# Performance work log

Hardware: AMD Instinct MI355X
Metric: run time of the kernel (lower is better)

Reference implementation:

```python
import jax, jax.numpy as jnp
import numpy as np

B, T, D_IN = 1024, 512, 32   # batch, sequence_length, input_dim
H = 512                      # hidden_dim
P = 96                       # prediction_length
D_OUT = 1                    # output_dim


def setup_inputs() -> dict:
    key = jax.random.key(0)
    ks = jax.random.split(key, 24)
    s = 1.0 / np.sqrt(H)  # PyTorch GRU default init scale
    u = lambda k, shape: jax.random.uniform(k, shape, jnp.float32, -s, s)
    inp = {"x": jax.random.normal(ks[0], (B, T, D_IN), jnp.float32)}
    # Encoder GRU: layer0 input D_IN, layer1 input H. Gate order: r, z, n.
    inp["enc_Wih0"] = u(ks[1], (3 * H, D_IN)); inp["enc_Whh0"] = u(ks[2], (3 * H, H))
    inp["enc_bih0"] = u(ks[3], (3 * H,));      inp["enc_bhh0"] = u(ks[4], (3 * H,))
    inp["enc_Wih1"] = u(ks[5], (3 * H, H));    inp["enc_Whh1"] = u(ks[6], (3 * H, H))
    inp["enc_bih1"] = u(ks[7], (3 * H,));      inp["enc_bhh1"] = u(ks[8], (3 * H,))
    # Decoder GRU: layer0 input D_OUT, layer1 input H.
    inp["dec_Wih0"] = u(ks[9], (3 * H, D_OUT)); inp["dec_Whh0"] = u(ks[10], (3 * H, H))
    inp["dec_bih0"] = u(ks[11], (3 * H,));      inp["dec_bhh0"] = u(ks[12], (3 * H,))
    inp["dec_Wih1"] = u(ks[13], (3 * H, H));    inp["dec_Whh1"] = u(ks[14], (3 * H, H))
    inp["dec_bih1"] = u(ks[15], (3 * H,));      inp["dec_bhh1"] = u(ks[16], (3 * H,))
    # Output projection + learned decoder start token.
    inp["out_W"] = u(ks[17], (D_OUT, H)); inp["out_b"] = u(ks[18], (D_OUT,))
    inp["dec_start"] = jnp.zeros((1, 1, D_OUT), jnp.float32)
    return inp


def gru_cell(x, h, Wih, Whh, bih, bhh):
    # PyTorch GRU cell: r,z,n gate order.
    gi = x @ Wih.T + bih          # [B, 3H]
    gh = h @ Whh.T + bhh          # [B, 3H]
    ir, iz, inn = jnp.split(gi, 3, axis=-1)
    hr, hz, hn = jnp.split(gh, 3, axis=-1)
    r = jax.nn.sigmoid(ir + hr)
    z = jax.nn.sigmoid(iz + hz)
    n = jnp.tanh(inn + r * hn)
    return (1.0 - z) * n + z * h


def reference(x,
              enc_Wih0, enc_Whh0, enc_bih0, enc_bhh0,
              enc_Wih1, enc_Whh1, enc_bih1, enc_bhh1,
              dec_Wih0, dec_Whh0, dec_bih0, dec_bhh0,
              dec_Wih1, dec_Whh1, dec_bih1, dec_bhh1,
              out_W, out_b, dec_start):
    Bsz = x.shape[0]
    h0 = jnp.zeros((Bsz, H), x.dtype)

    def enc_step(carry, xt):
        h1, h2 = carry
        h1 = gru_cell(xt, h1, enc_Wih0, enc_Whh0, enc_bih0, enc_bhh0)
        h2 = gru_cell(h1, h2, enc_Wih1, enc_Whh1, enc_bih1, enc_bhh1)
        return (h1, h2), None

    (h1, h2), _ = jax.lax.scan(enc_step, (h0, h0), jnp.swapaxes(x, 0, 1))

    y0 = jnp.broadcast_to(dec_start[0], (Bsz, D_OUT)).astype(x.dtype)

    def dec_step(carry, _):
        d1, d2, y = carry
        d1 = gru_cell(y, d1, dec_Wih0, dec_Whh0, dec_bih0, dec_bhh0)
        d2 = gru_cell(d1, d2, dec_Wih1, dec_Whh1, dec_bih1, dec_bhh1)
        y = d2 @ out_W.T + out_b  # [B, D_OUT]
        return (d1, d2, y), y

    _, ys = jax.lax.scan(dec_step, (h1, h2, y0), None, length=P)
    return jnp.swapaxes(ys, 0, 1)  # [B, P, D_OUT]
```

## Files before the change

### kernel.cpp

```cpp
#include <hip/hip_runtime.h>

#define HD 512
#define BB 1024
#define TT 512
#define PP 96
#define DIN 32
#define KC_H 16
#define NBLK 256
#define GRPB 16

typedef unsigned short u16;
typedef __attribute__((ext_vector_type(8))) short bf16x8;
typedef __attribute__((ext_vector_type(4))) float f32x4;
typedef __attribute__((address_space(3))) unsigned int lds_u32;
typedef __attribute__((address_space(3))) u16 lds_u16;
typedef __attribute__((address_space(1))) unsigned int glb_u32;

#define WAIT_VM(N) asm volatile("s_waitcnt vmcnt(" #N ")" ::: "memory")
__device__ __forceinline__ void bar_raw() { asm volatile("s_barrier" ::: "memory"); }

template <int N> __device__ __forceinline__ void wvm() {
  if constexpr (N == 0) WAIT_VM(0);
  else if constexpr (N == 2) WAIT_VM(2);
  else if constexpr (N == 4) WAIT_VM(4);
  else if constexpr (N == 5) WAIT_VM(5);
  else if constexpr (N == 10) WAIT_VM(10);
  else if constexpr (N == 13) WAIT_VM(13);
}

__device__ __forceinline__ float bf2f(u16 s) {
  return __uint_as_float(((unsigned)s) << 16);
}
__device__ __forceinline__ u16 f2bf_rne(float f) {
  unsigned u = __float_as_uint(f);
  u += 0x7FFF + ((u >> 16) & 1);
  return (u16)(u >> 16);
}
__device__ __forceinline__ float sigm(float v) { return 1.f / (1.f + __expf(-v)); }
__device__ __forceinline__ float tanh_(float a) {
  return 1.f - 2.f / (__expf(2.f * a) + 1.f);
}

__device__ __forceinline__ bf16x8 load_sc16(const u16* p) {
  bf16x8 r;
  asm volatile("global_load_dwordx4 %0, %1, off sc0 sc1" : "=&v"(r) : "v"(p) : "memory");
  return r;
}
__device__ __forceinline__ void store_sc_u16(u16* p, unsigned v) {
  asm volatile("global_store_short %0, %1, off sc0 sc1" :: "v"(p), "v"(v) : "memory");
}
__device__ __forceinline__ void store_sc_f32(float* p, float v) {
  asm volatile("global_store_dword %0, %1, off sc0 sc1" :: "v"(p), "v"(v) : "memory");
}
__device__ __forceinline__ float load_sc_f32w(const float* p) {
  float v;
  asm volatile("global_load_dword %0, %1, off sc0 sc1\ns_waitcnt vmcnt(0)"
               : "=&v"(v) : "v"(p) : "memory");
  return v;
}
__device__ __forceinline__ unsigned load_sc_u32w(const unsigned* p) {
  unsigned v;
  asm volatile("global_load_dword %0, %1, off sc0 sc1\ns_waitcnt vmcnt(0)"
               : "=&v"(v) : "v"(p) : "memory");
  return v;
}
__device__ __forceinline__ void store_h_sc(u16* H, u16* L, size_t idx, float hv) {
  u16 hi = (u16)(__float_as_uint(hv) >> 16);
  u16 lo = f2bf_rne(hv - bf2f(hi));
  store_sc_u16(H + idx, (unsigned)hi);
  store_sc_u16(L + idx, (unsigned)lo);
}


__global__ void pack_w_kernel(const float* __restrict__ W, int K,
                              u16* __restrict__ out) {
  int tid = blockIdx.x * 256 + threadIdx.x;
  int KC = K >> 5;
  int total = 16 * KC * 2 * 6 * 64;
  if (tid >= total) return;
  int lane = tid & 63;
  int rest = tid >> 6;
  int gs = rest % 6; rest /= 6;
  int fc = rest & 1; rest >>= 1;
  int kc = rest % KC;
  int jb = rest / KC;
  int g = gs >> 1, s = gs & 1;
  int j = jb * 32 + fc * 16 + (lane & 15);
  int k = kc * 32 + (lane >> 4) * 8;
  const float* src = W + (size_t)(g * HD + j) * K + k;
  bf16x8 v;
#pragma unroll
  for (int i = 0; i < 8; ++i) {
    float f = src[i];
    u16 hi = f2bf_rne(f);
    v[i] = (short)((s == 0) ? hi : f2bf_rne(f - bf2f(hi)));
  }
  *(bf16x8*)(out + (size_t)tid * 8) = v;
}

template <int NA> struct AFN { bf16x8 h[NA]; bf16x8 l[NA]; };
template <int NA>
__device__ __forceinline__ void fence_afn(AFN<NA>& a) {
#pragma unroll
  for (int n = 0; n < NA; ++n)
    asm volatile("" : "+v"(a.h[n]), "+v"(a.l[n]));
}

__device__ __forceinline__ void mfma_kc9(const lds_u16* base, int lane,
                                         bf16x8 ah, bf16x8 al,
                                         f32x4& R, f32x4& Z, f32x4& N) {
  typedef __attribute__((address_space(3))) const bf16x8 lds_bf16x8;
  const lds_u16* p = base + lane * 8;
#pragma unroll
  for (int g = 0; g < 3; ++g) {
    f32x4* a = (g == 0) ? &R : (g == 1) ? &Z : &N;
    bf16x8 whi = *(lds_bf16x8*)(p + (g * 2 + 0) * 512);
    bf16x8 wlo = *(lds_bf16x8*)(p + (g * 2 + 1) * 512);
    *a = __builtin_amdgcn_mfma_f32_16x16x32_bf16(ah, whi, *a, 0, 0, 0);
    *a = __builtin_amdgcn_mfma_f32_16x16x32_bf16(al, whi, *a, 0, 0, 0);
    *a = __builtin_amdgcn_mfma_f32_16x16x32_bf16(ah, wlo, *a, 0, 0, 0);
  }
}
__device__ __forceinline__ void mfma_kc9_g(const u16* base, int lane,
                                           bf16x8 ah, bf16x8 al,
                                           f32x4& R, f32x4& Z, f32x4& N) {
  const u16* p = base + lane * 8;
#pragma unroll
  for (int g = 0; g < 3; ++g) {
    f32x4* a = (g == 0) ? &R : (g == 1) ? &Z : &N;
    bf16x8 whi = *(const bf16x8*)(p + (g * 2 + 0) * 512);
    bf16x8 wlo = *(const bf16x8*)(p + (g * 2 + 1) * 512);
    *a = __builtin_amdgcn_mfma_f32_16x16x32_bf16(ah, whi, *a, 0, 0, 0);
    *a = __builtin_amdgcn_mfma_f32_16x16x32_bf16(al, whi, *a, 0, 0, 0);
    *a = __builtin_amdgcn_mfma_f32_16x16x32_bf16(ah, wlo, *a, 0, 0, 0);
  }
}

template <int NS>
__device__ __forceinline__ void piece_map(const u16* const (&Wjb)[NS],
                                          int lane, int wave,
                                          const u16* (&srcB)[NS * 3],
                                          int (&dstO)[NS * 3]) {
#pragma unroll
  for (int i = 0; i < NS * 3; ++i) {
    const int p = wave * (NS * 3) + i;
    const int s = p / 12, r = p % 12, f2 = r / 6, j = r % 6;
    const int co = f2 * 3072 + j * 512;
    srcB[i] = Wjb[s] + co + lane * 8;
    dstO[i] = s * 6144 + co;
  }
}

template <int NS>
__device__ __forceinline__ void stageW2(u16* ringb, const u16* const (&Wjb)[NS],
                                        int lane, int wave) {
  const u16* srcB[NS * 3]; int dstO[NS * 3];
  piece_map<NS>(Wjb, lane, wave, srcB, dstO);
#pragma unroll
  for (int ikc = 0; ikc < 2; ++ikc)
#pragma unroll
    for (int i = 0; i < NS * 3; ++i)
      __builtin_amdgcn_global_load_lds(
          (const glb_u32*)(srcB[i] + (size_t)ikc * 6144),
          (lds_u32*)(ringb + (size_t)ikc * NS * 6144 + dstO[i]), 16, 0, 0);
}

template <int NS, int NA>
__device__ __forceinline__ void pipePre(
    u16* ringb,
    const u16* const (&Ahi)[NA], const u16* const (&Alo)[NA],
    const u16* const (&Wjb)[NS], const int (&ai)[NS],
    f32x4* (&acc)[NS][3],
    int row0w, int lane, int wave) {
  constexpr int B = NS * 3 + 2 * NA;
  constexpr int A2 = 2 * NA;
  constexpr int SLOT = NS * 6144;
  const int quad = lane >> 4, n16 = lane & 15;
  const u16* aH[NA]; const u16* aL[NA];
#pragma unroll
  for (int n = 0; n < NA; ++n) {
    const size_t base = (size_t)(row0w >> 4) * (KC_H * 512) + n16 * 32 + quad * 8;
    aH[n] = Ahi[n] + base;
    aL[n] = Alo[n] + base;
  }
  const u16* srcB[NS * 3]; int dstO[NS * 3];
  piece_map<NS>(Wjb, lane, wave, srcB, dstO);
  u16* pb[3] = {ringb, ringb + SLOT, ringb + 2 * SLOT};
  AFN<NA> af0, af1, af2;

  auto issueA = [&](int ikc, AFN<NA>& dst) {
#pragma unroll
    for (int n = 0; n < NA; ++n) {
      dst.h[n] = load_sc16(aH[n] + ikc * 512);
      dst.l[n] = load_sc16(aL[n] + ikc * 512);
    }
  };
  auto issueB = [&](int ikc, int si, AFN<NA>& dst) {
#pragma unroll
    for (int i = 0; i < NS * 3; ++i)
      __builtin_amdgcn_global_load_lds(
          (const glb_u32*)(srcB[i] + (size_t)ikc * 6144),
          (lds_u32*)(pb[si] + dstO[i]), 16, 0, 0);
    issueA(ikc, dst);
  };
  auto cons = [&](int si, AFN<NA>& a) {
    fence_afn(a);
#pragma unroll
    for (int s = 0; s < NS; ++s)
#pragma unroll
      for (int f = 0; f < 2; ++f)
        mfma_kc9((const lds_u16*)(pb[si] + s * 6144 + f * 3072), lane,
                 a.h[ai[s]], a.l[ai[s]],
                 acc[s][0][f], acc[s][1][f], acc[s][2][f]);
  };

  WAIT_VM(0);
  issueA(0, af0);
  issueA(1, af1);
  wvm<A2>(); bar_raw(); issueB(2, 2, af2); cons(0, af0);
  wvm<B>();  bar_raw(); issueB(3, 0, af0); cons(1, af1);
#pragma unroll 1
  for (int q = 0; q < 4; ++q) {
    const int base = 4 + q * 3;
    wvm<B>(); bar_raw(); issueB(base + 0, 1, af1); cons(2, af2);
    wvm<B>(); bar_raw(); issueB(base + 1, 2, af2); cons(0, af0);
    wvm<B>(); bar_raw(); issueB(base + 2, 0, af0); cons(1, af1);
  }
  wvm<B>(); bar_raw(); cons(2, af2);
  wvm<0>(); bar_raw(); cons(0, af0);
}

__device__ __forceinline__ void x_acc(const float* x, int t, const u16* Wp,
                                      int jb, int row0w, int lane,
                                      f32x4* aR, f32x4* aZ, f32x4* aN) {
  const int quad = lane >> 4, n16 = lane & 15;
  const float* xp = x + (size_t)(row0w + n16) * (TT * DIN) +
                    (size_t)t * DIN + quad * 8;
  f32x4 v0 = *(const f32x4*)xp;
  f32x4 v1 = *(const f32x4*)(xp + 4);
  bf16x8 hi, lo;
#pragma unroll
  for (int i = 0; i < 8; ++i) {
    float f = (i < 4) ? v0[i] : v1[i - 4];
    u16 h = (u16)(__float_as_uint(f) >> 16);
    hi[i] = (short)h;
    lo[i] = (short)f2bf_rne(f - bf2f(h));
  }
#pragma unroll
  for (int f = 0; f < 2; ++f)
    mfma_kc9_g(Wp + ((size_t)jb * 2 + f) * 3072, lane, hi, lo,
               aR[f], aZ[f], aN[f]);
}

__device__ __forceinline__ void gbar_arrive(unsigned* gen) {
  WAIT_VM(0);
  __syncthreads();
  if (threadIdx.x == 0) atomicAdd(gen, 1u);
}
__device__ __forceinline__ void gbar_wait(unsigned* gen, unsigned target) {
  if (threadIdx.x == 0) {
    while (load_sc_u32w(gen) < target) __builtin_amdgcn_s_sleep(2);
  }
  __syncthreads();
}

__device__ __forceinline__ void gru_epi_reg(
    const float* bi, const float* bh, float (*ht)[4],
    u16* hnH, u16* hnL, int jb, int col0, int row0w, int quad, int n16,
    const f32x4* aR, const f32x4* aZ, const f32x4* aNX, const f32x4* aNH) {
  const size_t hb = ((size_t)(row0w >> 4) * KC_H + jb) * 512;
#pragma unroll
  for (int f = 0; f < 2; ++f) {
    const int col = col0 + f * 16;
    const float bir = bi[col],          bhr = bh[col];
    const float biz = bi[HD + col],     bhz = bh[HD + col];
    const float bin = bi[2 * HD + col], bhn = bh[2 * HD + col];
#pragma unroll
    for (int r = 0; r < 4; ++r) {
      const size_t idx = hb + (quad * 4 + r) * 32 + f * 16 + n16;
      float rr = sigm(aR[f][r] + bir + bhr);
      float zz = sigm(aZ[f][r] + biz + bhz);
      float nn = tanh_(aNX[f][r] + bin + rr * (aNH[f][r] + bhn));
      float hv = (1.f - zz) * nn + zz * ht[f][r];
      ht[f][r] = hv;
      store_h_sc(hnH, hnL, idx, hv);
    }
  }
}

__global__ __launch_bounds__(256, 1)
void gru_persistent_kernel(
    const float* x,
    const u16* pkX0, const u16* pkH0, const float* bi0, const float* bh0,
    const u16* pkX1, const u16* pkH1, const float* bi1, const float* bh1,
    const u16* pkD0H, const float* dbi0, const float* dbh0, const float* dW0,
    const u16* pkD1I, const u16* pkD1H, const float* dbi1, const float* dbh1,
    const float* outW, const float* outb, const float* dstart,
    u16* h1aH, u16* h1aL, u16* h1bH, u16* h1bL,
    u16* h2aH, u16* h2aL, u16* h2bH, u16* h2bL,
    float* yfull, float* dout, unsigned* gen) {
  __shared__ u16 ring[3 * 3 * 6144];
  const int b = blockIdx.x;
  const int jb = (b & 7) * 2 + ((b >> 3) & 1);
  const int row0 = (b >> 4) * 64;
  const int tid = threadIdx.x, wave = tid >> 6, lane = tid & 63;
  const int quad = lane >> 4, n16 = lane & 15;
  const int row0w = row0 + wave * 16;
  const int col0 = jb * 32 + n16;
  u16* ringb = &ring[0];
  const f32x4 z4 = {0.f, 0.f, 0.f, 0.f};
  const size_t jbs = (size_t)jb * (KC_H * 2 * 3072);
  const u16* pkH0j = pkH0 + jbs;
  const u16* pkX1j = pkX1 + jbs;
  const u16* pkH1j = pkH1 + jbs;
  const u16* pkD0Hj = pkD0H + jbs;
  const u16* pkD1Ij = pkD1I + jbs;
  const u16* pkD1Hj = pkD1H + jbs;
  unsigned* geng = gen + ((b >> 4) << 6);

  u16 *h1cH = h1aH, *h1cL = h1aL, *h1nH = h1bH, *h1nL = h1bL;
  u16 *h2cH = h2aH, *h2cL = h2aL, *h2nH = h2bH, *h2nL = h2bL;
  float ht1[2][4] = {{0, 0, 0, 0}, {0, 0, 0, 0}};
  float ht2[2][4] = {{0, 0, 0, 0}, {0, 0, 0, 0}};
  unsigned it = 0;

  f32x4 xR[2] = {z4, z4}, xZ[2] = {z4, z4}, xN[2] = {z4, z4};
  {
    const u16* Wv1[1] = {pkH0j};
    stageW2<1>(ringb, Wv1, lane, wave);
    x_acc(x, 0, pkX0, jb, row0w, lane, xR, xZ, xN);
  }

  for (int k = 0; k <= TT; ++k) {
    f32x4 R0[2], Z0[2], NX0[2], NH0[2] = {z4, z4};
    f32x4 R1[2] = {z4, z4}, Z1[2] = {z4, z4}, NX1[2] = {z4, z4}, NH1[2] = {z4, z4};
    if (k < TT) {
      R0[0] = xR[0]; R0[1] = xR[1];
      Z0[0] = xZ[0]; Z0[1] = xZ[1];
      NX0[0] = xN[0]; NX0[1] = xN[1];
    } else {
      R0[0] = z4; R0[1] = z4; Z0[0] = z4; Z0[1] = z4; NX0[0] = z4; NX0[1] = z4;
    }
    if (k > 0 && k < TT) {
      const u16* Ah[2] = {h1cH, h2cH};
      const u16* Al[2] = {h1cL, h2cL};
      const u16* Wv[3] = {pkH0j, pkX1j, pkH1j};
      const int ai3[3] = {0, 0, 1};
      f32x4* ac[3][3] = {{R0, Z0, NH0}, {R1, Z1, NX1}, {R1, Z1, NH1}};
      pipePre<3, 2>(ringb, Ah, Al, Wv, ai3, ac, row0w, lane, wave);
    } else if (k == 0) {
      const u16* Ah[1] = {h1cH};
      const u16* Al[1] = {h1cL};
      const u16* Wv[1] = {pkH0j};
      const int ai1[1] = {0};
      f32x4* ac[1][3] = {{R0, Z0, NH0}};
      pipePre<1, 1>(ringb, Ah, Al, Wv, ai1, ac, row0w, lane, wave);
    } else {
      const u16* Ah[2] = {h1cH, h2cH};
      const u16* Al[2] = {h1cL, h2cL};
      const u16* Wv[2] = {pkX1j, pkH1j};
      const int ai2[2] = {0, 1};
      f32x4* ac[2][3] = {{R1, Z1, NX1}, {R1, Z1, NH1}};
      pipePre<2, 2>(ringb, Ah, Al, Wv, ai2, ac, row0w, lane, wave);
    }
    if (k < TT)
      gru_epi_reg(bi0, bh0, ht1, h1nH, h1nL, jb, col0, row0w, quad, n16,
                  R0, Z0, NX0, NH0);
    if (k > 0)
      gru_epi_reg(bi1, bh1, ht2, h2nH, h2nL, jb, col0, row0w, quad, n16,
                  R1, Z1, NX1, NH1);
    ++it;
    gbar_arrive(geng);
    if (k + 1 < TT) {
      xR[0] = z4; xR[1] = z4; xZ[0] = z4; xZ[1] = z4; xN[0] = z4; xN[1] = z4;
      x_acc(x, k + 1, pkX0, jb, row0w, lane, xR, xZ, xN);
    }
    if (k + 1 < TT) {
      const u16* Wv3[3] = {pkH0j, pkX1j, pkH1j};
      stageW2<3>(ringb, Wv3, lane, wave);
    } else if (k + 1 == TT) {
      const u16* Wv2[2] = {pkX1j, pkH1j};
      stageW2<2>(ringb, Wv2, lane, wave);
    } else {
      const u16* Wv1[1] = {pkD0Hj};
      stageW2<1>(ringb, Wv1, lane, wave);
    }
    gbar_wait(geng, GRPB * it);
    if (k < TT) { u16* t0 = h1cH; h1cH = h1nH; h1nH = t0;
                  u16* t1 = h1cL; h1cL = h1nL; h1nL = t1; }
    if (k > 0)  { u16* t0 = h2cH; h2cH = h2nH; h2nH = t0;
                  u16* t1 = h2cL; h2cL = h2nL; h2nL = t1; }
  }

  for (int t = 0; t < PP; ++t) {
    {
      f32x4 R[2] = {z4, z4}, Z[2] = {z4, z4}, NH[2] = {z4, z4};
      {
        const u16* Ah[1] = {h1cH};
        const u16* Al[1] = {h1cL};
        const u16* Wv[1] = {pkD0Hj};
        const int ai1[1] = {0};
        f32x4* ac[1][3] = {{R, Z, NH}};
        pipePre<1, 1>(ringb, Ah, Al, Wv, ai1, ac, row0w, lane, wave);
      }
      float yl[4] = {0, 0, 0, 0};
      if (t > 0) {
        const float* yb = yfull + ((t - 1) & 1) * BB;
#pragma unroll
        for (int r = 0; r < 4; ++r) {
          const float* p = yb + (row0w + quad * 4 + r);
          asm volatile("global_load_dword %0, %1, off sc0 sc1"
                       : "=&v"(yl[r]) : "v"(p) : "memory");
        }
        WAIT_VM(0);
#pragma unroll
        for (int r = 0; r < 4; ++r)
          asm volatile("" : "+v"(yl[r]));
      }
      const float ds0 = dstart[0], ob0 = outb[0];
      const size_t hb = ((size_t)(row0w >> 4) * KC_H + jb) * 512;
#pragma unroll
      for (int f = 0; f < 2; ++f) {
        const int col = col0 + f * 16;
        const float bir = dbi0[col],          bhr = dbh0[col];
        const float biz = dbi0[HD + col],     bhz = dbh0[HD + col];
        const float bin = dbi0[2 * HD + col], bhn = dbh0[2 * HD + col];
        const float w0r = dW0[col], w0z = dW0[HD + col], w0n = dW0[2 * HD + col];
#pragma unroll
        for (int r = 0; r < 4; ++r) {
          const int row = row0w + quad * 4 + r;
          const size_t idx = hb + (quad * 4 + r) * 32 + f * 16 + n16;
          float yv = (t == 0) ? ds0 : (ob0 + yl[r]);
          if (f == 0 && t > 0 && jb == 0 && n16 == 0)
            dout[(size_t)row * PP + (t - 1)] = yv;
          float rr = sigm(R[f][r] + bir + bhr + yv * w0r);
          float zz = sigm(Z[f][r] + biz + bhz + yv * w0z);
          float nn = tanh_(bin + yv * w0n + rr * (NH[f][r] + bhn));
          float hv = (1.f - zz) * nn + zz * ht1[f][r];
          ht1[f][r] = hv;
          store_h_sc(h1nH, h1nL, idx, hv);
        }
      }
    }
    ++it;
    gbar_arrive(geng);
    {
      const u16* Wv2[2] = {pkD1Ij, pkD1Hj};
      stageW2<2>(ringb, Wv2, lane, wave);
    }
    gbar_wait(geng, GRPB * it);
    {
      f32x4 R[2] = {z4, z4}, Z[2] = {z4, z4}, NX[2] = {z4, z4}, NH[2] = {z4, z4};
      {
        const u16* Ah[2] = {h1nH, h2cH};
        const u16* Al[2] = {h1nL, h2cL};
        const u16* Wv[2] = {pkD1Ij, pkD1Hj};
        const int ai2[2] = {0, 1};
        f32x4* ac[2][3] = {{R, Z, NX}, {R, Z, NH}};
        pipePre<2, 2>(ringb, Ah, Al, Wv, ai2, ac, row0w, lane, wave);
      }
      float vs[4] = {0, 0, 0, 0};
      const size_t hb = ((size_t)(row0w >> 4) * KC_H + jb) * 512;
#pragma unroll
      for (int f = 0; f < 2; ++f) {
        const int col = col0 + f * 16;
        const float bir = dbi1[col],          bhr = dbh1[col];
        const float biz = dbi1[HD + col],     bhz = dbh1[HD + col];
        const float bin = dbi1[2 * HD + col], bhn = dbh1[2 * HD + col];
        const float wo = outW[col];
#pragma unroll
        for (int r = 0; r < 4; ++r) {
          const size_t idx = hb + (quad * 4 + r) * 32 + f * 16 + n16;
          float rr = sigm(R[f][r] + bir + bhr);
          float zz = sigm(Z[f][r] + biz + bhz);
          float nn = tanh_(NX[f][r] + bin + rr * (NH[f][r] + bhn));
          float hv = (1.f - zz) * nn + zz * ht2[f][r];
          ht2[f][r] = hv;
          store_h_sc(h2nH, h2nL, idx, hv);
          float v = hv * wo;
#pragma unroll
          for (int off = 1; off < 16; off <<= 1) v += __shfl_xor(v, off, 16);
          vs[r] += v;
        }
      }
      float* yw = yfull + (t & 1) * BB;
      float* yz = yfull + ((t - 1) & 1) * BB;
#pragma unroll
      for (int r = 0; r < 4; ++r) {
        const int row = row0w + quad * 4 + r;
        if (n16 == 0) {
          atomicAdd(yw + row, vs[r]);
          if (t > 0 && jb == 0) store_sc_f32(yz + row, 0.f);
        }
      }
    }
    ++it;
    gbar_arrive(geng);
    if (t + 1 < PP) {
      const u16* Wv1[1] = {pkD0Hj};
      stageW2<1>(ringb, Wv1, lane, wave);
    }
    gbar_wait(geng, GRPB * it);
    { u16* t0 = h1cH; h1cH = h1nH; h1nH = t0;
      u16* t1 = h1cL; h1cL = h1nL; h1nL = t1; }
    { u16* t0 = h2cH; h2cH = h2nH; h2nH = t0;
      u16* t1 = h2cL; h2cL = h2nL; h2nL = t1; }
  }

  if ((b & 15) == 0 && tid < 64) {
    int row = row0 + tid;
    float v = load_sc_f32w(yfull + ((PP - 1) & 1) * BB + row);
    dout[(size_t)row * PP + (PP - 1)] = outb[0] + v;
  }
}

extern "C" void kernel_launch(void* const* d_in, const int* in_sizes, int n_in,
                              void* d_out, int out_size, void* d_ws, size_t ws_size,
                              hipStream_t stream) {
  const float* x      = (const float*)d_in[0];
  const float* eW_ih0 = (const float*)d_in[1];
  const float* eW_hh0 = (const float*)d_in[2];
  const float* eb_ih0 = (const float*)d_in[3];
  const float* eb_hh0 = (const float*)d_in[4];
  const float* eW_ih1 = (const float*)d_in[5];
  const float* eW_hh1 = (const float*)d_in[6];
  const float* eb_ih1 = (const float*)d_in[7];
  const float* eb_hh1 = (const float*)d_in[8];
  const float* dW_ih0 = (const float*)d_in[9];
  const float* dW_hh0 = (const float*)d_in[10];
  const float* db_ih0 = (const float*)d_in[11];
  const float* db_hh0 = (const float*)d_in[12];
  const float* dW_ih1 = (const float*)d_in[13];
  const float* dW_hh1 = (const float*)d_in[14];
  const float* db_ih1 = (const float*)d_in[15];
  const float* db_hh1 = (const float*)d_in[16];
  const float* outW   = (const float*)d_in[17];
  const float* outb   = (const float*)d_in[18];
  const float* dstart = (const float*)d_in[19];
  float* out = (float*)d_out;

  char* w = (char*)d_ws;
  size_t off = 0;
  auto carve = [&](size_t bytes) -> void* {
    void* p = w + off;
    off = (off + bytes + 255) & ~(size_t)255;
    return p;
  };
  u16* h1aH = (u16*)carve((size_t)BB * HD * 2); u16* h1aL = (u16*)carve((size_t)BB * HD * 2);
  u16* h1bH = (u16*)carve((size_t)BB * HD * 2); u16* h1bL = (u16*)carve((size_t)BB * HD * 2);
  u16* h2aH = (u16*)carve((size_t)BB * HD * 2); u16* h2aL = (u16*)carve((size_t)BB * HD * 2);
  u16* h2bH = (u16*)carve((size_t)BB * HD * 2); u16* h2bL = (u16*)carve((size_t)BB * HD * 2);
  float* yfull = (float*)carve((size_t)2 * BB * 4);
  unsigned* gen = (unsigned*)carve(4096);
  auto carve_pack = [&](int K) -> u16* {
    return (u16*)carve((size_t)3 * HD * K * 2 * 2);
  };
  u16* pk_e0ih = carve_pack(DIN);
  u16* pk_e0hh = carve_pack(HD);
  u16* pk_e1ih = carve_pack(HD);
  u16* pk_e1hh = carve_pack(HD);
  u16* pk_d0hh = carve_pack(HD);
  u16* pk_d1ih = carve_pack(HD);
  u16* pk_d1hh = carve_pack(HD);

  hipMemsetAsync(h1aH, 0, (size_t)BB * HD * 2, stream);
  hipMemsetAsync(h1aL, 0, (size_t)BB * HD * 2, stream);
  hipMemsetAsync(h2aH, 0, (size_t)BB * HD * 2, stream);
  hipMemsetAsync(h2aL, 0, (size_t)BB * HD * 2, stream);
  hipMemsetAsync(yfull, 0, (size_t)2 * BB * 4, stream);
  hipMemsetAsync(gen, 0, 4096, stream);

  auto pack = [&](const float* W, int K, u16* dst) {
    int total = 16 * (K >> 5) * 2 * 6 * 64;
    pack_w_kernel<<<(total + 255) / 256, 256, 0, stream>>>(W, K, dst);
  };
  pack(eW_ih0, DIN, pk_e0ih);
  pack(eW_hh0, HD, pk_e0hh);
  pack(eW_ih1, HD, pk_e1ih);
  pack(eW_hh1, HD, pk_e1hh);
  pack(dW_hh0, HD, pk_d0hh);
  pack(dW_ih1, HD, pk_d1ih);
  pack(dW_hh1, HD, pk_d1hh);

  gru_persistent_kernel<<<NBLK, 256, 0, stream>>>(
      x, pk_e0ih, pk_e0hh, eb_ih0, eb_hh0,
      pk_e1ih, pk_e1hh, eb_ih1, eb_hh1,
      pk_d0hh, db_ih0, db_hh0, dW_ih0,
      pk_d1ih, pk_d1hh, db_ih1, db_hh1,
      outW, outb, dstart,
      h1aH, h1aL, h1bH, h1bL, h2aH, h2aL, h2bH, h2bL,
      yfull, out, gen);
}
```

Before: 15.84 ms.

## Assign block roles by XCD so row groups share L2 and relax cache scope

Blocks read their XCC ID at startup and claim roles so that all 16 blocks of a row group land on the same XCD when possible, with a two-phase global handshake to hand out any leftover roles. When a group turns out to be XCD-local, the hidden-state loads and stores drop the sc1 (system/device-coherent) bit and use only sc0, so traffic can stay in the shared L2 instead of going further out. This aims to cut cross-XCD coherence latency on the per-step recurrent state exchange. In exchange it adds startup spin barriers and atomics, and correctness now depends on the XCD-locality detection being right.

```diff
diff --git a/kernel.cpp b/kernel.cpp
--- a/kernel.cpp
+++ b/kernel.cpp
@@ -41,13 +41,20 @@
   return 1.f - 2.f / (__expf(2.f * a) + 1.f);
 }
 
-__device__ __forceinline__ bf16x8 load_sc16(const u16* p) {
+template <bool LOC>
+__device__ __forceinline__ bf16x8 load_a16(const u16* p) {
   bf16x8 r;
-  asm volatile("global_load_dwordx4 %0, %1, off sc0 sc1" : "=&v"(r) : "v"(p) : "memory");
+  if constexpr (LOC)
+    asm volatile("global_load_dwordx4 %0, %1, off sc0" : "=&v"(r) : "v"(p) : "memory");
+  else
+    asm volatile("global_load_dwordx4 %0, %1, off sc0 sc1" : "=&v"(r) : "v"(p) : "memory");
   return r;
 }
-__device__ __forceinline__ void store_sc_u16(u16* p, unsigned v) {
-  asm volatile("global_store_short %0, %1, off sc0 sc1" :: "v"(p), "v"(v) : "memory");
+__device__ __forceinline__ void store_h_u16(u16* p, unsigned v, bool loc) {
+  if (loc)
+    asm volatile("global_store_short %0, %1, off sc0" :: "v"(p), "v"(v) : "memory");
+  else
+    asm volatile("global_store_short %0, %1, off sc0 sc1" :: "v"(p), "v"(v) : "memory");
 }
 __device__ __forceinline__ void store_sc_f32(float* p, float v) {
   asm volatile("global_store_dword %0, %1, off sc0 sc1" :: "v"(p), "v"(v) : "memory");
@@ -64,11 +71,12 @@
                : "=&v"(v) : "v"(p) : "memory");
   return v;
 }
-__device__ __forceinline__ void store_h_sc(u16* H, u16* L, size_t idx, float hv) {
+__device__ __forceinline__ void store_h_sc(u16* H, u16* L, size_t idx, float hv,
+                                           bool loc) {
   u16 hi = (u16)(__float_as_uint(hv) >> 16);
   u16 lo = f2bf_rne(hv - bf2f(hi));
-  store_sc_u16(H + idx, (unsigned)hi);
-  store_sc_u16(L + idx, (unsigned)lo);
+  store_h_u16(H + idx, (unsigned)hi, loc);
+  store_h_u16(L + idx, (unsigned)lo, loc);
 }
 
 
@@ -165,7 +173,7 @@
           (lds_u32*)(ringb + (size_t)ikc * NS * 6144 + dstO[i]), 16, 0, 0);
 }
 
-template <int NS, int NA>
+template <int NS, int NA, bool LOC>
 __device__ __forceinline__ void pipePre(
     u16* ringb,
     const u16* const (&Ahi)[NA], const u16* const (&Alo)[NA],
@@ -191,8 +199,8 @@
   auto issueA = [&](int ikc, AFN<NA>& dst) {
 #pragma unroll
     for (int n = 0; n < NA; ++n) {
-      dst.h[n] = load_sc16(aH[n] + ikc * 512);
-      dst.l[n] = load_sc16(aL[n] + ikc * 512);
+      dst.h[n] = load_a16<LOC>(aH[n] + ikc * 512);
+      dst.l[n] = load_a16<LOC>(aL[n] + ikc * 512);
     }
   };
   auto issueB = [&](int ikc, int si, AFN<NA>& dst) {
@@ -267,6 +275,7 @@
 __device__ __forceinline__ void gru_epi_reg(
     const float* bi, const float* bh, float (*ht)[4],
     u16* hnH, u16* hnL, int jb, int col0, int row0w, int quad, int n16,
+    bool loc,
     const f32x4* aR, const f32x4* aZ, const f32x4* aNX, const f32x4* aNH) {
   const size_t hb = ((size_t)(row0w >> 4) * KC_H + jb) * 512;
 #pragma unroll
@@ -283,7 +292,7 @@
       float nn = tanh_(aNX[f][r] + bin + rr * (aNH[f][r] + bhn));
       float hv = (1.f - zz) * nn + zz * ht[f][r];
       ht[f][r] = hv;
-      store_h_sc(hnH, hnL, idx, hv);
+      store_h_sc(hnH, hnL, idx, hv, loc);
     }
   }
 }
@@ -298,13 +307,46 @@
     const float* outW, const float* outb, const float* dstart,
     u16* h1aH, u16* h1aL, u16* h1bH, u16* h1bL,
     u16* h2aH, u16* h2aL, u16* h2bH, u16* h2bL,
-    float* yfull, float* dout, unsigned* gen) {
+    float* yfull, float* dout, unsigned* gen,
+    unsigned* ictr, unsigned* xclaim, unsigned* taken, unsigned* gmask) {
   __shared__ u16 ring[3 * 3 * 6144];
-  const int b = blockIdx.x;
-  const int jb = (b & 7) * 2 + ((b >> 3) & 1);
-  const int row0 = (b >> 4) * 64;
+  __shared__ int meta[4];
   const int tid = threadIdx.x, wave = tid >> 6, lane = tid & 63;
   const int quad = lane >> 4, n16 = lane & 15;
+
+  if (tid == 0) {
+    unsigned xcd;
+    asm volatile("s_getreg_b32 %0, hwreg(HW_REG_XCC_ID)" : "=s"(xcd));
+    xcd &= 7;
+    unsigned s = atomicAdd(xclaim + xcd * 64, 1u);
+    int role = -1;
+    if (s < 32) {
+      role = (int)(((2u * xcd + (s >> 4)) << 4) | (s & 15u));
+      atomicExch(taken + role, 1u);
+      atomicOr(gmask + (role >> 4) * 64, 1u << xcd);
+    }
+    atomicAdd(ictr, 1u);
+    while (load_sc_u32w(ictr) < NBLK) __builtin_amdgcn_s_sleep(2);
+    if (role < 0) {
+      int r = 0;
+      for (;;) {
+        if (load_sc_u32w(taken + r) == 0u &&
+            atomicCAS(taken + r, 0u, 1u) == 0u) { role = r; break; }
+        r = (r + 1) & 255;
+      }
+      atomicOr(gmask + (role >> 4) * 64, 0x100u);
+    }
+    atomicAdd(ictr, 1u);
+    while (load_sc_u32w(ictr) < 2 * NBLK) __builtin_amdgcn_s_sleep(2);
+    unsigned m = load_sc_u32w(gmask + (role >> 4) * 64);
+    meta[2] = role;
+    meta[3] = (__popc(m & 0xFFu) == 1 && !(m & 0x100u)) ? 1 : 0;
+  }
+  __syncthreads();
+  const int role = meta[2];
+  const bool loc = meta[3] != 0;
+  const int jb = role & 15;
+  const int row0 = (role >> 4) * 64;
   const int row0w = row0 + wave * 16;
   const int col0 = jb * 32 + n16;
   u16* ringb = &ring[0];
@@ -316,7 +358,7 @@
   const u16* pkD0Hj = pkD0H + jbs;
   const u16* pkD1Ij = pkD1I + jbs;
   const u16* pkD1Hj = pkD1H + jbs;
-  unsigned* geng = gen + ((b >> 4) << 6);
+  unsigned* geng = gen + (role >> 4) * 64;
 
   u16 *h1cH = h1aH, *h1cL = h1aL, *h1nH = h1bH, *h1nL = h1bL;
   u16 *h2cH = h2aH, *h2cL = h2aL, *h2nH = h2bH, *h2nL = h2bL;
@@ -347,27 +389,30 @@
       const u16* Wv[3] = {pkH0j, pkX1j, pkH1j};
       const int ai3[3] = {0, 0, 1};
       f32x4* ac[3][3] = {{R0, Z0, NH0}, {R1, Z1, NX1}, {R1, Z1, NH1}};
-      pipePre<3, 2>(ringb, Ah, Al, Wv, ai3, ac, row0w, lane, wave);
+      if (loc) pipePre<3, 2, true>(ringb, Ah, Al, Wv, ai3, ac, row0w, lane, wave);
+      else     pipePre<3, 2, false>(ringb, Ah, Al, Wv, ai3, ac, row0w, lane, wave);
     } else if (k == 0) {
       const u16* Ah[1] = {h1cH};
       const u16* Al[1] = {h1cL};
       const u16* Wv[1] = {pkH0j};
       const int ai1[1] = {0};
       f32x4* ac[1][3] = {{R0, Z0, NH0}};
-      pipePre<1, 1>(ringb, Ah, Al, Wv, ai1, ac, row0w, lane, wave);
+      if (loc) pipePre<1, 1, true>(ringb, Ah, Al, Wv, ai1, ac, row0w, lane, wave);
+      else     pipePre<1, 1, false>(ringb, Ah, Al, Wv, ai1, ac, row0w, lane, wave);
     } else {
       const u16* Ah[2] = {h1cH, h2cH};
       const u16* Al[2] = {h1cL, h2cL};
       const u16* Wv[2] = {pkX1j, pkH1j};
       const int ai2[2] = {0, 1};
       f32x4* ac[2][3] = {{R1, Z1, NX1}, {R1, Z1, NH1}};
-      pipePre<2, 2>(ringb, Ah, Al, Wv, ai2, ac, row0w, lane, wave);
+      if (loc) pipePre<2, 2, true>(ringb, Ah, Al, Wv, ai2, ac, row0w, lane, wave);
+      else     pipePre<2, 2, false>(ringb, Ah, Al, Wv, ai2, ac, row0w, lane, wave);
     }
     if (k < TT)
-      gru_epi_reg(bi0, bh0, ht1, h1nH, h1nL, jb, col0, row0w, quad, n16,
+      gru_epi_reg(bi0, bh0, ht1, h1nH, h1nL, jb, col0, row0w, quad, n16, loc,
                   R0, Z0, NX0, NH0);
     if (k > 0)
-      gru_epi_reg(bi1, bh1, ht2, h2nH, h2nL, jb, col0, row0w, quad, n16,
+      gru_epi_reg(bi1, bh1, ht2, h2nH, h2nL, jb, col0, row0w, quad, n16, loc,
                   R1, Z1, NX1, NH1);
     ++it;
     gbar_arrive(geng);
@@ -401,7 +446,8 @@
         const u16* Wv[1] = {pkD0Hj};
         const int ai1[1] = {0};
         f32x4* ac[1][3] = {{R, Z, NH}};
-        pipePre<1, 1>(ringb, Ah, Al, Wv, ai1, ac, row0w, lane, wave);
+        if (loc) pipePre<1, 1, true>(ringb, Ah, Al, Wv, ai1, ac, row0w, lane, wave);
+        else     pipePre<1, 1, false>(ringb, Ah, Al, Wv, ai1, ac, row0w, lane, wave);
       }
       float yl[4] = {0, 0, 0, 0};
       if (t > 0) {
@@ -438,7 +484,7 @@
           float nn = tanh_(bin + yv * w0n + rr * (NH[f][r] + bhn));
           float hv = (1.f - zz) * nn + zz * ht1[f][r];
           ht1[f][r] = hv;
-          store_h_sc(h1nH, h1nL, idx, hv);
+          store_h_sc(h1nH, h1nL, idx, hv, loc);
         }
       }
     }
@@ -457,7 +503,8 @@
         const u16* Wv[2] = {pkD1Ij, pkD1Hj};
         const int ai2[2] = {0, 1};
         f32x4* ac[2][3] = {{R, Z, NX}, {R, Z, NH}};
-        pipePre<2, 2>(ringb, Ah, Al, Wv, ai2, ac, row0w, lane, wave);
+        if (loc) pipePre<2, 2, true>(ringb, Ah, Al, Wv, ai2, ac, row0w, lane, wave);
+        else     pipePre<2, 2, false>(ringb, Ah, Al, Wv, ai2, ac, row0w, lane, wave);
       }
       float vs[4] = {0, 0, 0, 0};
       const size_t hb = ((size_t)(row0w >> 4) * KC_H + jb) * 512;
@@ -476,7 +523,7 @@
           float nn = tanh_(NX[f][r] + bin + rr * (NH[f][r] + bhn));
           float hv = (1.f - zz) * nn + zz * ht2[f][r];
           ht2[f][r] = hv;
-          store_h_sc(h2nH, h2nL, idx, hv);
+          store_h_sc(h2nH, h2nL, idx, hv, loc);
           float v = hv * wo;
 #pragma unroll
           for (int off = 1; off < 16; off <<= 1) v += __shfl_xor(v, off, 16);
@@ -507,7 +554,7 @@
       u16* t1 = h2cL; h2cL = h2nL; h2nL = t1; }
   }
 
-  if ((b & 15) == 0 && tid < 64) {
+  if (jb == 0 && tid < 64) {
     int row = row0 + tid;
     float v = load_sc_f32w(yfull + ((PP - 1) & 1) * BB + row);
     dout[(size_t)row * PP + (PP - 1)] = outb[0] + v;
@@ -552,6 +599,10 @@
   u16* h2bH = (u16*)carve((size_t)BB * HD * 2); u16* h2bL = (u16*)carve((size_t)BB * HD * 2);
   float* yfull = (float*)carve((size_t)2 * BB * 4);
   unsigned* gen = (unsigned*)carve(4096);
+  unsigned* ictr = (unsigned*)carve(256);
+  unsigned* xclaim = (unsigned*)carve(2048);
+  unsigned* taken = (unsigned*)carve(1024);
+  unsigned* gmask = (unsigned*)carve(4096);
   auto carve_pack = [&](int K) -> u16* {
     return (u16*)carve((size_t)3 * HD * K * 2 * 2);
   };
@@ -569,6 +620,10 @@
   hipMemsetAsync(h2aL, 0, (size_t)BB * HD * 2, stream);
   hipMemsetAsync(yfull, 0, (size_t)2 * BB * 4, stream);
   hipMemsetAsync(gen, 0, 4096, stream);
+  hipMemsetAsync(ictr, 0, 256, stream);
+  hipMemsetAsync(xclaim, 0, 2048, stream);
+  hipMemsetAsync(taken, 0, 1024, stream);
+  hipMemsetAsync(gmask, 0, 4096, stream);
 
   auto pack = [&](const float* W, int K, u16* dst) {
     int total = 16 * (K >> 5) * 2 * 6 * 64;
@@ -589,5 +644,5 @@
       pk_d1ih, pk_d1hh, db_ih1, db_hh1,
       outW, outb, dstart,
       h1aH, h1aL, h1bH, h1bL, h2aH, h2aL, h2bH, h2bL,
-      yfull, out, gen);
-}
+      yfull, out, gen, ictr, xclaim, taken, gmask);
+}
```

Result: slower. 20.65 ms (+30.4%).
